# Performance work log

Measured on AMD Instinct MI355X. Metric: run time of the kernel, lower is better.

Reference implementation:

```python
import jax, jax.numpy as jnp
import numpy as np

NBINS = 256
STRENGTH = 100.0
C, H, W = 64, 512, 512


def setup_inputs() -> dict:
    key = jax.random.key(0)
    k1, k2, k3, k4 = jax.random.split(key, 4)
    inp = jax.random.uniform(k1, (1, C, H, W), dtype=jnp.float32)
    tgt = jax.random.uniform(k2, (1, C, H, W), dtype=jnp.float32)
    maskI = jax.random.randint(k3, (1, 1, H, W), 0, 2).astype(jnp.int32)
    maskJ = jax.random.randint(k4, (1, 1, H, W), 0, 2).astype(jnp.int32)
    return {"input": inp, "target": tgt, "maskI": maskI, "maskJ": maskJ}


def _hist_remap(I, J, mI, mJ):
    # I, J: [c, HW] float; mI, mJ: [HW] {0,1} float
    c, hw = I.shape
    nI = mI.sum()
    nJ = mJ.sum()
    big = jnp.float32(1e30)
    # per-channel min/max of masked target values (J[mJ].view(c, nJ).min/max)
    minJ = jnp.min(jnp.where(mJ > 0, J, big), axis=1)   # [c]
    maxJ = jnp.max(jnp.where(mJ > 0, J, -big), axis=1)  # [c]
    step = (maxJ - minJ) / NBINS                          # [c]
    # masked per-channel histogram of target (cu.histogram), scaled by nI/nJ
    binJ = jnp.clip(jnp.floor((J - minJ[:, None]) / jnp.maximum(step[:, None], 1e-12)),
                    0, NBINS - 1).astype(jnp.int32)
    seg = binJ + jnp.arange(c, dtype=jnp.int32)[:, None] * NBINS
    hisJ = jax.ops.segment_sum(jnp.broadcast_to(mJ, (c, hw)).reshape(-1),
                               seg.reshape(-1), num_segments=c * NBINS).reshape(c, NBINS)
    hisJ = hisJ * (nI / nJ)
    cumJ = jnp.cumsum(hisJ, axis=1)                       # [c, nbins]
    # mask input; unmasked pixels -> -1 so they sort to the front (msk_sub trick)
    _I = I * mI - (1.0 - mI)                              # [c, HW]
    idxI = jnp.argsort(_I, axis=1)                        # ascending sort order
    # 1-indexed rank among the nI masked pixels (unmasked ranks <= 0, ignored later)
    rank = jnp.arange(hw, dtype=jnp.float32) - (hw - nI) + 1.0  # [HW]

    def per_ch(cum, his, r, mn, st):
        # CDF inverse: smallest bin b with cum[b] >= rank (cu.hist_remap2)
        b = jnp.clip(jnp.searchsorted(cum, r, side='left'), 0, NBINS - 1)
        lo = cum[b] - his[b]
        ratio = jnp.clip((r - lo) / jnp.maximum(his[b], 1e-12), 0.0, 1.0)
        return mn + (b.astype(jnp.float32) + ratio) * st

    vals = jax.vmap(per_ch)(cumJ, hisJ, jnp.broadcast_to(rank, (c, hw)), minJ, step)  # [c, HW]
    # scatter remapped sorted values back to original pixel positions
    R_sorted = jax.vmap(lambda idx, v: jnp.zeros(hw, dtype=v.dtype).at[idx].set(v))(idxI, vals)
    R = jnp.where(mI > 0, R_sorted, I)
    return R


def reference(input, target, maskI, maskJ):
    _, c, h, w = input.shape
    hw = h * w
    I = input[0].reshape(c, hw)
    J = target[0].reshape(c, hw)
    mI = maskI[0, 0].reshape(hw).astype(jnp.float32)
    mJ = maskJ[0, 0].reshape(hw).astype(jnp.float32)
    R = _hist_remap(I, J, mI, mJ)
    # F.mse_loss(I, R) * strength
    loss = jnp.mean((I - R) ** 2) * STRENGTH
    return loss
```

## Files before the change

kernel.cpp:

```cpp
#include <hip/hip_runtime.h>


#define CN    64
#define HWN   262144
#define NB    256
#define NBUK  8192
#define NBLK  16
#define BPIX  (HWN/NBLK)
#define PT    512
#define MMS   64
#define MMPIX (HWN/MMS)
#define CLB   32
#define CBUK  (NBUK/CLB)
#define FXS2  268435456.0f
#define FXSI2 (1.0/268435456.0)

__global__ __launch_bounds__(512) void k_prep(
    const float* __restrict__ J, const int* __restrict__ mI,
    const int* __restrict__ mJ, unsigned char* __restrict__ bI,
    unsigned char* __restrict__ bJ, unsigned* __restrict__ mnp,
    unsigned* __restrict__ mxp, double* __restrict__ lossacc,
    unsigned* __restrict__ donecnt)
{
  const int bx = blockIdx.x, tid = threadIdx.x;
  __shared__ unsigned smn[8][8], smx[8][8];
  if(bx < 64){
    const int t = bx*512 + tid;
    const int4* a = (const int4*)mI + 2*t;
    int4 x0 = a[0], x1 = a[1];
    unsigned b = (unsigned)((x0.x>0)|((x0.y>0)<<1)|((x0.z>0)<<2)|((x0.w>0)<<3)
               |((x1.x>0)<<4)|((x1.y>0)<<5)|((x1.z>0)<<6)|((x1.w>0)<<7));
    const int4* cm = (const int4*)mJ + 2*t;
    int4 y0 = cm[0], y1 = cm[1];
    unsigned d = (unsigned)((y0.x>0)|((y0.y>0)<<1)|((y0.z>0)<<2)|((y0.w>0)<<3)
               |((y1.x>0)<<4)|((y1.y>0)<<5)|((y1.z>0)<<6)|((y1.w>0)<<7));
    bI[t] = (unsigned char)b;
    bJ[t] = (unsigned char)d;
    if(bx == 0 && tid == 0){ *lossacc = 0.0; *donecnt = 0u; }
    return;
  }
  const int m = bx - 64, s = m >> 3, g = m & 7;
  const int wid = tid >> 6, lane = tid & 63;
  const int4* mj4 = (const int4*)mJ + s*(MMPIX/4);
  int4 y0 = mj4[tid], y1 = mj4[512 + tid];
  unsigned b40 = (unsigned)((y0.x>0)|((y0.y>0)<<1)|((y0.z>0)<<2)|((y0.w>0)<<3));
  unsigned b41 = (unsigned)((y1.x>0)|((y1.y>0)<<1)|((y1.z>0)<<2)|((y1.w>0)<<3));
  #pragma unroll
  for(int ch = 0; ch < 8; ch++){
    const int c = g*8 + ch;
    const float4* Jc = (const float4*)(J + (size_t)c*HWN + (size_t)s*MMPIX);
    float4 v0 = Jc[tid], v1 = Jc[512 + tid];
    unsigned mn = 0x7F800000u, mx = 0u;
    if(b40&1u){unsigned u=__float_as_uint(v0.x); mn=min(mn,u); mx=max(mx,u);}
    if(b40&2u){unsigned u=__float_as_uint(v0.y); mn=min(mn,u); mx=max(mx,u);}
    if(b40&4u){unsigned u=__float_as_uint(v0.z); mn=min(mn,u); mx=max(mx,u);}
    if(b40&8u){unsigned u=__float_as_uint(v0.w); mn=min(mn,u); mx=max(mx,u);}
    if(b41&1u){unsigned u=__float_as_uint(v1.x); mn=min(mn,u); mx=max(mx,u);}
    if(b41&2u){unsigned u=__float_as_uint(v1.y); mn=min(mn,u); mx=max(mx,u);}
    if(b41&4u){unsigned u=__float_as_uint(v1.z); mn=min(mn,u); mx=max(mx,u);}
    if(b41&8u){unsigned u=__float_as_uint(v1.w); mn=min(mn,u); mx=max(mx,u);}
    for(int o = 32; o > 0; o >>= 1){
      mn = min(mn, (unsigned)__shfl_down(mn, o, 64));
      mx = max(mx, (unsigned)__shfl_down(mx, o, 64));
    }
    if(lane == 0){ smn[wid][ch] = mn; smx[wid][ch] = mx; }
  }
  __syncthreads();
  if(tid < 8){
    unsigned mn = 0x7F800000u, mx = 0u;
    for(int w = 0; w < 8; w++){ mn = min(mn, smn[w][tid]); mx = max(mx, smx[w][tid]); }
    mnp[(g*8 + tid)*MMS + s] = mn;
    mxp[(g*8 + tid)*MMS + s] = mx;
  }
}

__device__ __forceinline__ void px_i(float v, float& qacc, unsigned& ci,
                                     unsigned* buk){
  int k = (int)(v * (float)NBUK);
  if(k > NBUK-1) k = NBUK-1;
  float dv = v - ((float)k + 0.5f) * (1.0f/(float)NBUK);
  int fx = (int)rintf(dv * FXS2);
  atomicAdd(&buk[k], ((unsigned)fx << 12) + 1u);
  qacc += dv*dv;
  ci++;
}

__global__ __launch_bounds__(PT, 2) void k_p1h(
    const float* __restrict__ I, const float* __restrict__ J,
    const unsigned* __restrict__ bIw, const unsigned* __restrict__ bJw,
    const unsigned* __restrict__ mnp, const unsigned* __restrict__ mxp,
    unsigned* __restrict__ pc, unsigned* __restrict__ qtot,
    unsigned* __restrict__ hisPart, unsigned* __restrict__ cp,
    double* __restrict__ qp)
{
  const int c = blockIdx.y, q = blockIdx.x, tid = threadIdx.x;
  const int bid = c*NBLK + q;
  const int wid = tid >> 6, lane = tid & 63;
  __shared__ unsigned buk[NBUK];
  __shared__ unsigned smbI[BPIX/32], smbJ[BPIX/32];
  __shared__ unsigned h2[2][NB];
  __shared__ double   dred[PT/64];
  __shared__ unsigned uci[PT/64], ucj[PT/64];
  __shared__ float sh_mn, sh_den;
  for(int i = tid; i < NBUK; i += PT) buk[i] = 0u;
  smbI[tid] = bIw[q*512 + tid];
  smbJ[tid] = bJw[q*512 + tid];
  if(tid < NB){ h2[0][tid] = 0u; h2[1][tid] = 0u; }
  if(tid < MMS){
    unsigned mn = mnp[c*MMS + tid];
    unsigned mx = mxp[c*MMS + tid];
    for(int o = 32; o > 0; o >>= 1){
      mn = min(mn, (unsigned)__shfl_down(mn, o, 64));
      mx = max(mx, (unsigned)__shfl_down(mx, o, 64));
    }
    if(tid == 0){
      float mnv = __uint_as_float(mn);
      sh_mn  = mnv;
      sh_den = fmaxf((__uint_as_float(mx) - mnv) / (float)NB, 1e-12f);
    }
  }
  __syncthreads();

  const float4* Ic = (const float4*)(I + (size_t)c*HWN + (size_t)q*BPIX);
  const float4* Jc = (const float4*)(J + (size_t)c*HWN + (size_t)q*BPIX);
  const float mnv = sh_mn, den = sh_den;
  float qacc = 0.0f;
  unsigned ci = 0, cj = 0;
  const int nsh = (tid & 7) * 4;
  const int bw  = tid >> 3;
  unsigned* hh = h2[wid & 1];

  float4 pi[2], pj[2];
  pi[0] = Ic[tid]; pj[0] = Jc[tid];
  #pragma unroll
  for(int g = 0; g < 8; g++){
    const int cur = g & 1, nxt = cur ^ 1;
    if(g < 7){ pi[nxt] = Ic[(g+1)*PT + tid]; pj[nxt] = Jc[(g+1)*PT + tid]; }
    const unsigned bitsI = (smbI[g*64 + bw] >> nsh) & 0xFu;
    const unsigned bitsJ = (smbJ[g*64 + bw] >> nsh) & 0xFu;
    float4 vi = pi[cur], vj = pj[cur];
    if(bitsI & 1u) px_i(vi.x, qacc, ci, buk);
    if(bitsI & 2u) px_i(vi.y, qacc, ci, buk);
    if(bitsI & 4u) px_i(vi.z, qacc, ci, buk);
    if(bitsI & 8u) px_i(vi.w, qacc, ci, buk);
    if(bitsJ & 1u){ float bf = floorf((vj.x - mnv)/den);
      bf = fminf(fmaxf(bf,0.0f),255.0f); atomicAdd(&hh[(int)bf],1u); cj++; }
    if(bitsJ & 2u){ float bf = floorf((vj.y - mnv)/den);
      bf = fminf(fmaxf(bf,0.0f),255.0f); atomicAdd(&hh[(int)bf],1u); cj++; }
    if(bitsJ & 4u){ float bf = floorf((vj.z - mnv)/den);
      bf = fminf(fmaxf(bf,0.0f),255.0f); atomicAdd(&hh[(int)bf],1u); cj++; }
    if(bitsJ & 8u){ float bf = floorf((vj.w - mnv)/den);
      bf = fminf(fmaxf(bf,0.0f),255.0f); atomicAdd(&hh[(int)bf],1u); cj++; }
  }
  __syncthreads();
  { unsigned* pcb = pc + (size_t)bid * NBUK;
    for(int i = tid; i < NBUK; i += PT) pcb[i] = buk[i]; }
  if(tid < NB) hisPart[(size_t)bid*NB + tid] = h2[0][tid] + h2[1][tid];

  { unsigned csum = 0;
    #pragma unroll
    for(int j = 0; j < 16; j++) csum += buk[tid*16 + j] & 0xFFFu;
    csum += __shfl_down(csum, 8, 64);
    csum += __shfl_down(csum, 4, 64);
    csum += __shfl_down(csum, 2, 64);
    csum += __shfl_down(csum, 1, 64);
    if((tid & 15) == 0) qtot[bid*32 + (tid >> 4)] = csum;
  }

  double qd = (double)qacc;
  for(int o = 32; o > 0; o >>= 1){
    qd += __shfl_down(qd, o, 64);
    ci += __shfl_down(ci, o, 64);
    cj += __shfl_down(cj, o, 64);
  }
  if(lane == 0){ dred[wid] = qd; uci[wid] = ci; ucj[wid] = cj; }
  __syncthreads();
  if(tid == 0){
    double t = 0.0; unsigned aci = 0, acj = 0;
    for(int w = 0; w < PT/64; w++){ t += dred[w]; aci += uci[w]; acj += ucj[w]; }
    qp[bid] = t;
    if(c == 0){ cp[2*q] = aci; cp[2*q+1] = acj; }
  }
}

__global__ __launch_bounds__(256) void k_closs(
    const unsigned* __restrict__ pc, const unsigned* __restrict__ qtot,
    const unsigned* __restrict__ hisPart,
    const unsigned* __restrict__ mnp, const unsigned* __restrict__ mxp,
    const unsigned* __restrict__ cp, const double* __restrict__ qp,
    double* __restrict__ lossacc, unsigned* __restrict__ donecnt,
    float* __restrict__ out)
{
  const int c = blockIdx.y, qt = blockIdx.x, tid = threadIdx.x;
  const int wid = tid >> 6, lane = tid & 63;
  __shared__ unsigned hsum[NB], qsh[NBLK*32];
  __shared__ float cs[NB], hs[NB];
  __shared__ unsigned colsum[32], wsum[4];
  __shared__ double red2[4];
  __shared__ float sh_mn, sh_st;
  __shared__ unsigned sh_base;

  if(tid < MMS){
    unsigned mn = mnp[c*MMS + tid];
    unsigned mx = mxp[c*MMS + tid];
    for(int o = 32; o > 0; o >>= 1){
      mn = min(mn, (unsigned)__shfl_down(mn, o, 64));
      mx = max(mx, (unsigned)__shfl_down(mx, o, 64));
    }
    if(tid == 0){
      float mnv = __uint_as_float(mn);
      sh_mn = mnv;
      sh_st = (__uint_as_float(mx) - mnv) / (float)NB;
    }
  }
  { unsigned hr = 0u;
    #pragma unroll
    for(int xb = 0; xb < NBLK; xb++) hr += hisPart[(size_t)(c*NBLK + xb)*NB + tid];
    hsum[tid] = hr; }
  qsh[tid]       = qtot[c*NBLK*32 + tid];
  qsh[tid + 256] = qtot[c*NBLK*32 + 256 + tid];
  __syncthreads();
  if(tid < 32){
    unsigned csm = 0;
    #pragma unroll
    for(int sl = 0; sl < NBLK; sl++) csm += qsh[sl*32 + tid];
    colsum[tid] = csm;
  }
  __syncthreads();
  if(tid == 0){
    unsigned ciw = 0, cjw = 0;
    for(int qi = 0; qi < NBLK; qi++){ ciw += cp[2*qi]; cjw += cp[2*qi+1]; }
    float ratio = (float)ciw / (float)cjw;
    float cum = 0.0f;
    for(int b = 0; b < NB; b++){
      float hh = (float)hsum[b] * ratio;
      hs[b] = hh;
      cum += hh;
      cs[b] = cum;
    }
    unsigned base = 0;
    for(int g2 = 0; g2 < qt; g2++) base += colsum[g2];
    sh_base = base;
  }
  __syncthreads();

  unsigned kk0=0, kk1=0, kk2=0, kk3=0;
  long long ss0=0, ss1=0, ss2=0, ss3=0;
  #pragma unroll
  for(int sl = 0; sl < NBLK; sl += 4){
    unsigned w0 = pc[(size_t)(c*NBLK + sl    )*NBUK + qt*CBUK + tid];
    unsigned w1 = pc[(size_t)(c*NBLK + sl + 1)*NBUK + qt*CBUK + tid];
    unsigned w2 = pc[(size_t)(c*NBLK + sl + 2)*NBUK + qt*CBUK + tid];
    unsigned w3 = pc[(size_t)(c*NBLK + sl + 3)*NBUK + qt*CBUK + tid];
    kk0 += w0 & 0xFFFu;  ss0 += (int)w0 >> 12;
    kk1 += w1 & 0xFFFu;  ss1 += (int)w1 >> 12;
    kk2 += w2 & 0xFFFu;  ss2 += (int)w2 >> 12;
    kk3 += w3 & 0xFFFu;  ss3 += (int)w3 >> 12;
  }
  unsigned  kk = kk0 + kk1 + kk2 + kk3;
  long long ss = ss0 + ss1 + ss2 + ss3;
  unsigned v = kk;
  for(int o = 1; o < 64; o <<= 1){
    unsigned t = __shfl_up(v, o, 64);
    if(lane >= o) v += t;
  }
  if(lane == 63) wsum[wid] = v;
  __syncthreads();
  unsigned wbase = 0;
  for(int w = 0; w < wid; w++) wbase += wsum[w];
  unsigned texcl = sh_base + wbase + (v - kk);

  float  mnvf = sh_mn, stepf = sh_st;
  double mnvd = (double)mnvf, stepd = (double)stepf;

  float rf0 = (float)(texcl + 1u);
  int lo = 0, hi = NB;
  while(lo < hi){ int mid = (lo + hi) >> 1; if(cs[mid] < rf0) lo = mid + 1; else hi = mid; }
  int bin = (lo > NB-1) ? NB-1 : lo;

  double acc = 0.0;
  if(kk){
    unsigned ra = texcl + 1u, rb = texcl + kk;
    double sval = 0.0;
    while(ra <= rb){
      while(bin < NB-1 && cs[bin] < (float)ra) bin++;
      float csb = cs[bin], hsb = hs[bin];
      unsigned re = (bin == NB-1) ? rb : min(rb, (unsigned)floorf(csb));
      double lovd = (double)csb - (double)hsb;
      double den2 = fmax((double)hsb, 1e-12);
      double ra_d = (double)ra, re_d = (double)re, nn = (double)(re - ra + 1u);
      double rta = (ra_d - lovd)/den2, rtb = (re_d - lovd)/den2;
      if(hsb > 0.0f && rta >= 0.0 && rtb <= 1.0){
        double sumr = 0.5*(ra_d + re_d)*nn;
        sval += nn*(mnvd + (double)bin*stepd) + stepd*(sumr - nn*lovd)/den2;
      } else {
        for(unsigned rr = ra; rr <= re; rr++){
          float rf = (float)rr;
          float lov = csb - hsb;
          float rt = (rf - lov) / fmaxf(hsb, 1e-12f);
          rt = fminf(fmaxf(rt, 0.0f), 1.0f);
          sval += (double)(mnvf + ((float)bin + rt)*stepf);
        }
      }
      ra = re + 1u;
    }
    double kb   = (double)kk;
    double cb   = ((double)(qt*CBUK + tid) + 0.5) * (1.0/(double)NBUK);
    double vbar = sval/kb - cb;
    double S    = (double)ss * FXSI2;
    acc = kb*vbar*vbar - 2.0*vbar*S;
  }
  if(qt == 0 && tid == 0){
    double qsum = 0.0;
    for(int qi = 0; qi < NBLK; qi++) qsum += qp[c*NBLK + qi];
    acc += qsum;
  }
  for(int o = 32; o > 0; o >>= 1) acc += __shfl_down(acc, o, 64);
  if(lane == 0) red2[wid] = acc;
  __syncthreads();
  if(tid == 0){
    double t = 0.0;
    for(int w = 0; w < 4; w++) t += red2[w];
    atomicAdd(lossacc, t);
    __threadfence();
    unsigned old = atomicAdd(donecnt, 1u);
    if(old == (unsigned)(CN*CLB - 1)){
      double tot = atomicAdd(lossacc, 0.0);
      out[0] = (float)(tot * (100.0 / (double)((size_t)CN * HWN)));
    }
  }
}

extern "C" void kernel_launch(void* const* d_in, const int* in_sizes, int n_in,
                              void* d_out, int out_size, void* d_ws, size_t ws_size,
                              hipStream_t stream){
  const float* I  = (const float*)d_in[0];
  const float* J  = (const float*)d_in[1];
  const int*   mI = (const int*)d_in[2];
  const int*   mJ = (const int*)d_in[3];
  float* out = (float*)d_out;

  char* base = (char*)d_ws;
  size_t pcB = (size_t)CN * NBLK * NBUK * sizeof(unsigned);
  unsigned* pc      = (unsigned*)base;
  char* p = base + pcB;
  double*   qp      = (double*)p;   p += (size_t)CN*NBLK*sizeof(double);
  double*   lossacc = (double*)p;   p += sizeof(double);
  unsigned* hisPart = (unsigned*)p; p += (size_t)CN*NBLK*NB*sizeof(unsigned);
  unsigned* qtot    = (unsigned*)p; p += (size_t)CN*NBLK*32*sizeof(unsigned);
  unsigned* mnp     = (unsigned*)p; p += (size_t)CN*MMS*sizeof(unsigned);
  unsigned* mxp     = (unsigned*)p; p += (size_t)CN*MMS*sizeof(unsigned);
  unsigned* cp      = (unsigned*)p; p += 2*NBLK*sizeof(unsigned);
  unsigned* donecnt = (unsigned*)p; p += sizeof(unsigned);
  size_t off = (size_t)(p - base); off = (off + 15) & ~(size_t)15;
  unsigned char* bIb = (unsigned char*)(base + off);
  unsigned char* bJb = bIb + HWN/8;

  k_prep<<<576, 512, 0, stream>>>(J, mI, mJ, bIb, bJb, mnp, mxp,
                                  lossacc, donecnt);
  k_p1h<<<dim3(NBLK, CN), PT, 0, stream>>>(I, J, (const unsigned*)bIb,
                                           (const unsigned*)bJb, mnp, mxp,
                                           pc, qtot, hisPart, cp, qp);
  k_closs<<<dim3(CLB, CN), 256, 0, stream>>>(pc, qtot, hisPart, mnp, mxp,
                                             cp, qp, lossacc, donecnt, out);
}
```

Baseline: 217.6 us.

## Split per-channel CDF table build into separate kernel and widen loss blocks

Adds a small k_tab kernel that builds each channel's scaled histogram, cumulative table, min/step and per-column rank prefixes once, so k_closs blocks no longer repeat the serial 256-bin cumsum and histogram reduction. k_closs now uses 512 threads and 16 column blocks per channel, loading the precomputed tables from global memory. This adds an extra kernel launch and a global round trip in exchange for removing redundant serial work in every loss block.

```diff
diff --git a/kernel.cpp b/kernel.cpp
--- a/kernel.cpp
+++ b/kernel.cpp
@@ -10,7 +10,7 @@
 #define PT    512
 #define MMS   64
 #define MMPIX (HWN/MMS)
-#define CLB   32
+#define CLB   16
 #define CBUK  (NBUK/CLB)
 #define FXS2  268435456.0f
 #define FXSI2 (1.0/268435456.0)
@@ -183,48 +183,39 @@
   }
 }
 
-__global__ __launch_bounds__(256) void k_closs(
-    const unsigned* __restrict__ pc, const unsigned* __restrict__ qtot,
-    const unsigned* __restrict__ hisPart,
+__global__ __launch_bounds__(256) void k_tab(
+    const unsigned* __restrict__ hisPart, const unsigned* __restrict__ qtot,
     const unsigned* __restrict__ mnp, const unsigned* __restrict__ mxp,
-    const unsigned* __restrict__ cp, const double* __restrict__ qp,
-    double* __restrict__ lossacc, unsigned* __restrict__ donecnt,
-    float* __restrict__ out)
+    const unsigned* __restrict__ cp,
+    float* __restrict__ chs, float* __restrict__ ccs,
+    float* __restrict__ cmn, float* __restrict__ cst,
+    unsigned* __restrict__ colpre)
 {
-  const int c = blockIdx.y, qt = blockIdx.x, tid = threadIdx.x;
-  const int wid = tid >> 6, lane = tid & 63;
-  __shared__ unsigned hsum[NB], qsh[NBLK*32];
-  __shared__ float cs[NB], hs[NB];
-  __shared__ unsigned colsum[32], wsum[4];
-  __shared__ double red2[4];
-  __shared__ float sh_mn, sh_st;
-  __shared__ unsigned sh_base;
-
-  if(tid < MMS){
-    unsigned mn = mnp[c*MMS + tid];
-    unsigned mx = mxp[c*MMS + tid];
-    for(int o = 32; o > 0; o >>= 1){
-      mn = min(mn, (unsigned)__shfl_down(mn, o, 64));
-      mx = max(mx, (unsigned)__shfl_down(mx, o, 64));
-    }
-    if(tid == 0){
-      float mnv = __uint_as_float(mn);
-      sh_mn = mnv;
-      sh_st = (__uint_as_float(mx) - mnv) / (float)NB;
-    }
-  }
+  const int c = blockIdx.x, tid = threadIdx.x;
+  __shared__ unsigned hsum[NB], colsum[32];
+  __shared__ float hsf[NB], csf[NB];
   { unsigned hr = 0u;
     #pragma unroll
     for(int xb = 0; xb < NBLK; xb++) hr += hisPart[(size_t)(c*NBLK + xb)*NB + tid];
     hsum[tid] = hr; }
-  qsh[tid]       = qtot[c*NBLK*32 + tid];
-  qsh[tid + 256] = qtot[c*NBLK*32 + 256 + tid];
-  __syncthreads();
   if(tid < 32){
-    unsigned csm = 0;
+    unsigned s = 0;
     #pragma unroll
-    for(int sl = 0; sl < NBLK; sl++) csm += qsh[sl*32 + tid];
-    colsum[tid] = csm;
+    for(int sl = 0; sl < NBLK; sl++) s += qtot[c*NBLK*32 + sl*32 + tid];
+    colsum[tid] = s;
+  }
+  if(tid >= 64 && tid < 128){
+    const int l = tid - 64;
+    unsigned mn = mnp[c*MMS + l], mx = mxp[c*MMS + l];
+    for(int o = 32; o > 0; o >>= 1){
+      mn = min(mn, (unsigned)__shfl_down(mn, o, 64));
+      mx = max(mx, (unsigned)__shfl_down(mx, o, 64));
+    }
+    if(l == 0){
+      float mnv = __uint_as_float(mn);
+      cmn[c] = mnv;
+      cst[c] = (__uint_as_float(mx) - mnv) / (float)NB;
+    }
   }
   __syncthreads();
   if(tid == 0){
@@ -234,15 +225,34 @@
     float cum = 0.0f;
     for(int b = 0; b < NB; b++){
       float hh = (float)hsum[b] * ratio;
-      hs[b] = hh;
+      hsf[b] = hh;
       cum += hh;
-      cs[b] = cum;
+      csf[b] = cum;
     }
     unsigned base = 0;
-    for(int g2 = 0; g2 < qt; g2++) base += colsum[g2];
-    sh_base = base;
-  }
-  __syncthreads();
+    for(int g = 0; g < 32; g++){ colpre[c*32 + g] = base; base += colsum[g]; }
+  }
+  __syncthreads();
+  chs[c*NB + tid] = hsf[tid];
+  ccs[c*NB + tid] = csf[tid];
+}
+
+__global__ __launch_bounds__(512) void k_closs(
+    const unsigned* __restrict__ pc, const float* __restrict__ chs,
+    const float* __restrict__ ccs, const float* __restrict__ cmn,
+    const float* __restrict__ cst, const unsigned* __restrict__ colpre,
+    const double* __restrict__ qp,
+    double* __restrict__ lossacc, unsigned* __restrict__ donecnt,
+    float* __restrict__ out)
+{
+  const int c = blockIdx.y, qt = blockIdx.x, tid = threadIdx.x;
+  const int wid = tid >> 6, lane = tid & 63;
+  __shared__ float cs[NB], hs[NB];
+  __shared__ unsigned wsum[8];
+  __shared__ double red2[8];
+  if(tid < NB){ cs[tid] = ccs[c*NB + tid]; hs[tid] = chs[c*NB + tid]; }
+  const float  mnvf = cmn[c], stepf = cst[c];
+  const unsigned base = colpre[c*32 + qt*2];
 
   unsigned kk0=0, kk1=0, kk2=0, kk3=0;
   long long ss0=0, ss1=0, ss2=0, ss3=0;
@@ -268,9 +278,8 @@
   __syncthreads();
   unsigned wbase = 0;
   for(int w = 0; w < wid; w++) wbase += wsum[w];
-  unsigned texcl = sh_base + wbase + (v - kk);
-
-  float  mnvf = sh_mn, stepf = sh_st;
+  unsigned texcl = base + wbase + (v - kk);
+
   double mnvd = (double)mnvf, stepd = (double)stepf;
 
   float rf0 = (float)(texcl + 1u);
@@ -320,7 +329,7 @@
   __syncthreads();
   if(tid == 0){
     double t = 0.0;
-    for(int w = 0; w < 4; w++) t += red2[w];
+    for(int w = 0; w < 8; w++) t += red2[w];
     atomicAdd(lossacc, t);
     __threadfence();
     unsigned old = atomicAdd(donecnt, 1u);
@@ -351,6 +360,11 @@
   unsigned* mnp     = (unsigned*)p; p += (size_t)CN*MMS*sizeof(unsigned);
   unsigned* mxp     = (unsigned*)p; p += (size_t)CN*MMS*sizeof(unsigned);
   unsigned* cp      = (unsigned*)p; p += 2*NBLK*sizeof(unsigned);
+  float*    chs     = (float*)p;    p += (size_t)CN*NB*sizeof(float);
+  float*    ccs     = (float*)p;    p += (size_t)CN*NB*sizeof(float);
+  float*    cmn     = (float*)p;    p += CN*sizeof(float);
+  float*    cst     = (float*)p;    p += CN*sizeof(float);
+  unsigned* colpre  = (unsigned*)p; p += (size_t)CN*32*sizeof(unsigned);
   unsigned* donecnt = (unsigned*)p; p += sizeof(unsigned);
   size_t off = (size_t)(p - base); off = (off + 15) & ~(size_t)15;
   unsigned char* bIb = (unsigned char*)(base + off);
@@ -361,6 +375,8 @@
   k_p1h<<<dim3(NBLK, CN), PT, 0, stream>>>(I, J, (const unsigned*)bIb,
                                            (const unsigned*)bJb, mnp, mxp,
                                            pc, qtot, hisPart, cp, qp);
-  k_closs<<<dim3(CLB, CN), 256, 0, stream>>>(pc, qtot, hisPart, mnp, mxp,
-                                             cp, qp, lossacc, donecnt, out);
-}
+  k_tab<<<CN, 256, 0, stream>>>(hisPart, qtot, mnp, mxp, cp,
+                                chs, ccs, cmn, cst, colpre);
+  k_closs<<<dim3(CLB, CN), 512, 0, stream>>>(pc, chs, ccs, cmn, cst, colpre,
+                                             qp, lossacc, donecnt, out);
+}
```

Result: faster. 186.2 us (-14.4%).
